# Optimization experiments

Hardware: AMD Instinct MI355X
Metric: run time of the kernel (lower is better)

The kernel has to match this reference:

```python
import jax, jax.numpy as jnp
import numpy as np

UNIF_T = 2.0
EPS = 1e-12  # matches F.normalize default eps


def _l2norm(a):
    return a / jnp.maximum(jnp.linalg.norm(a, axis=-1, keepdims=True), EPS)


def setup_inputs() -> dict:
    key = jax.random.key(0)
    k1, k2, k3, k4 = jax.random.split(key, 4)
    n, d = 2048, 512
    Q, K = 3, 8192
    n_classes = 16
    x = jax.random.normal(k1, (n, d), dtype=jnp.float32)
    q_data = jax.random.normal(k2, (Q, K, d), dtype=jnp.float32)
    targets = jax.random.randint(k3, (n,), 0, n_classes, dtype=jnp.int64)
    q_targets = jax.random.randint(k4, (Q, K), 0, n_classes, dtype=jnp.int64)
    return {"x": x, "q_data": q_data, "targets": targets, "q_targets": q_targets, "order": 1}


def reference(x, q_data, targets, q_targets, order):
    # x: [n, d], q_data: [Q, K, d], targets: [n], q_targets: [Q, K]
    Q, K, _ = q_data.shape
    xn = _l2norm(x)
    qn = _l2norm(q_data)
    sim = jnp.einsum('nd,qkd->qnk', xn, qn)      # [Q, n, K]
    e = jnp.exp(-UNIF_T * (2.0 - 2.0 * sim))     # [Q, n, K]
    # mask[i, j] = targets[i] == q_targets[order, j]; masked entries of the
    # `order` queue are excluded from that row's mean.
    mask = targets[:, None] == q_targets[order][None, :]   # [n, K] bool
    total = e.sum(axis=(0, 2))                              # [n]
    masked_sum = jnp.where(mask, e[order], 0.0).sum(axis=1) # [n]
    count = (Q * K - mask.sum(axis=1)).astype(e.dtype)      # [n]
    loss = jnp.mean(jnp.log((total - masked_sum) / count))
    return loss
```

## Files before the change

### kernel.cpp

```cpp
#include <hip/hip_runtime.h>
#include <cstdint>
#include <cstddef>

#define N_ROWS 2048
#define DIM    512
#define QN     3
#define KQ     8192
#define NCOL   (QN * KQ)
#define NCLASS 16

#define BM 256
#define BN 256
#define BKT 64
#define NT  (DIM / BKT)
#define NBLKP (NCOL / BN)

typedef __attribute__((ext_vector_type(4))) float f32x4;

__global__ __launch_bounds__(256) void norm_cast_kernel(
    const float* __restrict__ x, const float* __restrict__ q,
    unsigned char* __restrict__ xb, unsigned char* __restrict__ qb,
    float* __restrict__ out) {
    if (blockIdx.x == 0 && threadIdx.x == 0) out[0] = 0.f;
    int row = blockIdx.x * 4 + (threadIdx.x >> 6);
    int lane = threadIdx.x & 63;
    const float* src;
    unsigned char* dst;
    if (row < N_ROWS) {
        src = x + (size_t)row * DIM;
        dst = xb + (size_t)row * DIM;
    } else {
        src = q + (size_t)(row - N_ROWS) * DIM;
        dst = qb + (size_t)(row - N_ROWS) * DIM;
    }
    float4 v0 = ((const float4*)src)[lane * 2];
    float4 v1 = ((const float4*)src)[lane * 2 + 1];
    float ss = v0.x*v0.x + v0.y*v0.y + v0.z*v0.z + v0.w*v0.w
             + v1.x*v1.x + v1.y*v1.y + v1.z*v1.z + v1.w*v1.w;
    #pragma unroll
    for (int off = 1; off < 64; off <<= 1)
        ss += __shfl_xor(ss, off, 64);
    float inv = 16.0f / fmaxf(sqrtf(ss), 1e-12f);
    int w0 = __builtin_amdgcn_cvt_pk_fp8_f32(v0.x * inv, v0.y * inv, 0,  false);
    w0     = __builtin_amdgcn_cvt_pk_fp8_f32(v0.z * inv, v0.w * inv, w0, true);
    int w1 = __builtin_amdgcn_cvt_pk_fp8_f32(v1.x * inv, v1.y * inv, 0,  false);
    w1     = __builtin_amdgcn_cvt_pk_fp8_f32(v1.z * inv, v1.w * inv, w1, true);
    uint2 o; o.x = (unsigned)w0; o.y = (unsigned)w1;
    int r2 = (row >> 2) & 1;
    *(uint2*)(dst + ((lane * 8) ^ (r2 << 3))) = o;
}

#define MF(A_, B_, C_) C_ = __builtin_amdgcn_mfma_f32_16x16x32_fp8_fp8(A_, B_, C_, 0, 0, 0)

#define STAGE(h_) do {                                                          \
    const int t_ = (h_) >> 2, ht_ = (h_) & 3;                                   \
    const int chunk_ = (ht_ & 1) * 8 + wave;           \
    const int R_ = chunk_ * 16 + stR;                      \
    const int k0_ = t_ * BKT;                                                   \
    if (ht_ < 2) {                                                              \
        unsigned char* d_ = ((t_ & 1) ? As1 : As0) + chunk_ * 1024 + lane * 16; \
        __builtin_amdgcn_global_load_lds(                                       \
            (const __attribute__((address_space(1))) unsigned int*)             \
                (Xb + (size_t)(m0 + R_) * DIM + k0_ + stC),                     \
            (__attribute__((address_space(3))) unsigned int*)d_, 16, 0, 0);     \
    } else {                                                                    \
        unsigned char* d_ = ((t_ & 1) ? Bs1 : Bs0) + chunk_ * 1024 + lane * 16; \
        __builtin_amdgcn_global_load_lds(                                       \
            (const __attribute__((address_space(1))) unsigned int*)             \
                (Qb + (size_t)(n0 + R_) * DIM + k0_ + stC),                     \
            (__attribute__((address_space(3))) unsigned int*)d_, 16, 0, 0);     \
    }                                                                           \
} while (0)

__global__ __launch_bounds__(512) void gemm_epilogue_kernel(
    const unsigned char* __restrict__ Xb,
    const unsigned char* __restrict__ Qb,
    const int* __restrict__ targets,
    const int* __restrict__ q_targets,
    const int* __restrict__ order_p,
    float* __restrict__ P) {

    __shared__ unsigned char As0[BM * BKT];
    __shared__ unsigned char As1[BM * BKT];
    __shared__ unsigned char Bs0[BN * BKT];
    __shared__ unsigned char Bs1[BN * BKT];

    const int tid  = threadIdx.x;
    const int lane = tid & 63;
    const int wave = tid >> 6;
    const int wm = wave >> 2, wn = wave & 3;
    const int quad = lane >> 4;
    const int l15  = lane & 15;
    const int r2l  = (l15 >> 2) & 1;
    const int skey = ((l15 >> 1) & 1) * 2 + ((l15 >> 3) & 1);

    const int b    = blockIdx.x;
    const int xcd  = b & 7;
    const int g    = b >> 3;
    const int colb = (g >> 3) * 8 + xcd;
    const int rowb = g & 7;
    const int m0 = rowb * BM;
    const int n0 = colb * BN;

    f32x4 acc[8][4];
    #pragma unroll
    for (int i = 0; i < 8; i++)
        #pragma unroll
        for (int j = 0; j < 4; j++)
            acc[i][j] = (f32x4){0.f, 0.f, 0.f, 0.f};

    const int stR = lane >> 2;
    const int stC = ((lane & 3) ^ (((stR >> 1) & 1) * 2 + ((stR >> 3) & 1))) * 16;

    const int swh = ((quad & 1) ^ r2l) << 3;
    const int sw0 = ((((quad >> 1)    ) ^ skey) << 4) + swh;
    const int sw1 = ((((quad >> 1) + 2) ^ skey) << 4) + swh;

    #pragma unroll
    for (int h = 0; h < 7; ++h) STAGE(h);
    asm volatile("s_waitcnt vmcnt(3)" ::: "memory");
    __builtin_amdgcn_sched_barrier(0);
    __builtin_amdgcn_s_barrier();

    #pragma unroll
    for (int ph = 0; ph < 32; ++ph) {
        const int it = ph >> 3, p = ph & 7;
        const int tt = it * 2 + (p >> 2);
        const int q  = p & 3;
        const unsigned char* Ab = (tt & 1) ? As1 : As0;
        const unsigned char* Bb = (tt & 1) ? Bs1 : Bs0;
        const int mt0 = (q >> 1) * 4, ntb = (q & 1) * 2;

        long a0[2], a1[2], a2[2], a3[2], b0[2], b1[2];
        {
            const unsigned char* pA0 = Ab + (wm * 128 + (mt0 + 0) * 16 + l15) * BKT;
            const unsigned char* pA1 = Ab + (wm * 128 + (mt0 + 1) * 16 + l15) * BKT;
            const unsigned char* pA2 = Ab + (wm * 128 + (mt0 + 2) * 16 + l15) * BKT;
            const unsigned char* pA3 = Ab + (wm * 128 + (mt0 + 3) * 16 + l15) * BKT;
            a0[0] = *(const long*)(pA0 + sw0); a0[1] = *(const long*)(pA0 + sw1);
            a1[0] = *(const long*)(pA1 + sw0); a1[1] = *(const long*)(pA1 + sw1);
            a2[0] = *(const long*)(pA2 + sw0); a2[1] = *(const long*)(pA2 + sw1);
            a3[0] = *(const long*)(pA3 + sw0); a3[1] = *(const long*)(pA3 + sw1);
            const unsigned char* pB0 = Bb + (wn * 64 + (ntb + 0) * 16 + l15) * BKT;
            const unsigned char* pB1 = Bb + (wn * 64 + (ntb + 1) * 16 + l15) * BKT;
            b0[0] = *(const long*)(pB0 + sw0); b0[1] = *(const long*)(pB0 + sw1);
            b1[0] = *(const long*)(pB1 + sw0); b1[1] = *(const long*)(pB1 + sw1);
        }

        const int hs = 7 + ph;
        if (hs < 4 * NT) STAGE(hs);

        if (q == 3) {
            if (it == 3) asm volatile("s_waitcnt vmcnt(0)" ::: "memory");
            else         asm volatile("s_waitcnt vmcnt(3)" ::: "memory");
            __builtin_amdgcn_sched_barrier(0);
        }
        __builtin_amdgcn_s_barrier();

        __builtin_amdgcn_s_setprio(1);
        #pragma unroll
        for (int ks = 0; ks < 2; ++ks) {
            MF(a0[ks], b0[ks], acc[mt0 + 0][ntb + 0]);
            MF(a0[ks], b1[ks], acc[mt0 + 0][ntb + 1]);
            MF(a1[ks], b0[ks], acc[mt0 + 1][ntb + 0]);
            MF(a1[ks], b1[ks], acc[mt0 + 1][ntb + 1]);
            MF(a2[ks], b0[ks], acc[mt0 + 2][ntb + 0]);
            MF(a2[ks], b1[ks], acc[mt0 + 2][ntb + 1]);
            MF(a3[ks], b0[ks], acc[mt0 + 3][ntb + 0]);
            MF(a3[ks], b1[ks], acc[mt0 + 3][ntb + 1]);
        }
        __builtin_amdgcn_s_setprio(0);
        __builtin_amdgcn_s_barrier();
    }

    __syncthreads();
    float* red = (float*)&As0[0];

    const int ord  = order_p[0];
    const int qIdx = colb / (KQ / BN);
    const bool isOrd = (qIdx == ord);
    const int kbase = n0 - qIdx * KQ;

    int qtv[4] = {0, 0, 0, 0};
    if (isOrd) {
        #pragma unroll
        for (int nt = 0; nt < 4; nt++)
            qtv[nt] = q_targets[ord * KQ + kbase + wn * 64 + nt * 16 + l15];
    }

    #pragma unroll
    for (int mt = 0; mt < 8; mt++) {
        int rowl = wm * 128 + mt * 16 + quad * 4;
        int tg[4] = {0, 0, 0, 0};
        if (isOrd) {
            #pragma unroll
            for (int reg = 0; reg < 4; reg++) tg[reg] = targets[m0 + rowl + reg];
        }
        #pragma unroll
        for (int reg = 0; reg < 4; reg++) {
            float s = 0.f;
            #pragma unroll
            for (int nt = 0; nt < 4; nt++) {
                float v256 = acc[mt][nt][reg];
                float e = __expf(v256 * 0.015625f - 4.0f);
                if (isOrd && tg[reg] == qtv[nt]) e = 0.f;
                s += e;
            }
            s += __shfl_xor(s, 1, 64);
            s += __shfl_xor(s, 2, 64);
            s += __shfl_xor(s, 4, 64);
            s += __shfl_xor(s, 8, 64);
            if (l15 == 0)
                red[wn * 256 + rowl + reg] = s;
        }
    }
    __syncthreads();
    if (tid < 256)
        P[(size_t)colb * N_ROWS + m0 + tid] =
            red[tid] + red[256 + tid] + red[512 + tid] + red[768 + tid];
}

__global__ __launch_bounds__(256) void reduce_kernel(
    const float* __restrict__ P,
    const int* __restrict__ targets,
    const int* __restrict__ q_targets,
    const int* __restrict__ order_p,
    float* __restrict__ out) {
    __shared__ int hist[NCLASS];
    __shared__ float partial[4];
    int tid = threadIdx.x;
    int wave = tid >> 6, lane = tid & 63;
    if (tid < NCLASS) hist[tid] = 0;
    __syncthreads();
    int ord = order_p[0];

    int local[NCLASS];
    #pragma unroll
    for (int c = 0; c < NCLASS; c++) local[c] = 0;
    for (int i = tid; i < KQ; i += 256) {
        int v = q_targets[ord * KQ + i];
        #pragma unroll
        for (int c = 0; c < NCLASS; c++)
            local[c] += __popcll(__ballot(v == c));
    }
    if (lane == 0) {
        #pragma unroll
        for (int c = 0; c < NCLASS; c++)
            atomicAdd(&hist[c], local[c]);
    }
    __syncthreads();

    int r = blockIdx.x * 256 + tid;
    float total = 0.f;
    #pragma unroll 8
    for (int nb = 0; nb < NBLKP; nb++)
        total += P[(size_t)nb * N_ROWS + r];
    float cnt = (float)(QN * KQ - hist[targets[r]]);
    float v = logf(total / cnt);

    #pragma unroll
    for (int off = 1; off < 64; off <<= 1)
        v += __shfl_xor(v, off, 64);
    if (lane == 0) partial[wave] = v;
    __syncthreads();
    if (tid == 0)
        atomicAdd(out, (partial[0] + partial[1] + partial[2] + partial[3])
                       * (1.0f / (float)N_ROWS));
}

extern "C" void kernel_launch(void* const* d_in, const int* in_sizes, int n_in,
                              void* d_out, int out_size, void* d_ws, size_t ws_size,
                              hipStream_t stream) {
    const float* x         = (const float*)d_in[0];
    const float* q         = (const float*)d_in[1];
    const int*   targets   = (const int*)d_in[2];
    const int*   q_targets = (const int*)d_in[3];
    const int*   order     = (const int*)d_in[4];
    float* out = (float*)d_out;

    char* ws = (char*)d_ws;
    float* P = (float*)ws;
    unsigned char* Xb = (unsigned char*)(ws + (size_t)NBLKP * N_ROWS * 4);
    unsigned char* Qb = Xb + (size_t)N_ROWS * DIM;

    norm_cast_kernel<<<(N_ROWS + NCOL) / 4, 256, 0, stream>>>(x, q, Xb, Qb, out);

    gemm_epilogue_kernel<<<NBLKP * (N_ROWS / BM), 512, 0, stream>>>(
        Xb, Qb, targets, q_targets, order, P);

    reduce_kernel<<<N_ROWS / 256, 256, 0, stream>>>(P, targets, q_targets, order, out);
}
```

Baseline: 180.5 us.

## Restructure GEMM main loop into 16 larger phases with B fragments reused

Replaces the 32 small phases (each 8 MFMAs on a 4x2 sub-tile) with 16 phases of 32 MFMAs. Each K-tile's B fragments are loaded once into registers and reused across both M halves. This halves the number of block barriers and cuts redundant LDS reads of B, at the cost of more live registers. Two global-to-LDS stages are now issued per phase, which changes how the async copies and vmcnt waits are spaced.

```diff
diff --git a/kernel.cpp b/kernel.cpp
--- a/kernel.cpp
+++ b/kernel.cpp
@@ -72,6 +72,71 @@
     }                                                                           \
 } while (0)
 
+#define RD_A(AB, MT0) do {                                                      \
+    const unsigned char* p_;                                                    \
+    p_ = (AB) + (wm * 128 + ((MT0) + 0) * 16 + l15) * BKT;                      \
+    a0[0] = *(const long*)(p_ + sw0); a0[1] = *(const long*)(p_ + sw1);         \
+    p_ = (AB) + (wm * 128 + ((MT0) + 1) * 16 + l15) * BKT;                      \
+    a1[0] = *(const long*)(p_ + sw0); a1[1] = *(const long*)(p_ + sw1);         \
+    p_ = (AB) + (wm * 128 + ((MT0) + 2) * 16 + l15) * BKT;                      \
+    a2[0] = *(const long*)(p_ + sw0); a2[1] = *(const long*)(p_ + sw1);         \
+    p_ = (AB) + (wm * 128 + ((MT0) + 3) * 16 + l15) * BKT;                      \
+    a3[0] = *(const long*)(p_ + sw0); a3[1] = *(const long*)(p_ + sw1);         \
+} while (0)
+
+#define RD_B(BB) do {                                                           \
+    const unsigned char* p_;                                                    \
+    p_ = (BB) + (wn * 64 +  0 + l15) * BKT;                                     \
+    B0[0] = *(const long*)(p_ + sw0); B0[1] = *(const long*)(p_ + sw1);         \
+    p_ = (BB) + (wn * 64 + 16 + l15) * BKT;                                     \
+    B1[0] = *(const long*)(p_ + sw0); B1[1] = *(const long*)(p_ + sw1);         \
+    p_ = (BB) + (wn * 64 + 32 + l15) * BKT;                                     \
+    B2[0] = *(const long*)(p_ + sw0); B2[1] = *(const long*)(p_ + sw1);         \
+    p_ = (BB) + (wn * 64 + 48 + l15) * BKT;                                     \
+    B3[0] = *(const long*)(p_ + sw0); B3[1] = *(const long*)(p_ + sw1);         \
+} while (0)
+
+#define MFMA16(KS, MT0)                                                         \
+    MF(a0[KS], B0[KS], acc[(MT0)+0][0]); MF(a0[KS], B1[KS], acc[(MT0)+0][1]);   \
+    MF(a0[KS], B2[KS], acc[(MT0)+0][2]); MF(a0[KS], B3[KS], acc[(MT0)+0][3]);   \
+    MF(a1[KS], B0[KS], acc[(MT0)+1][0]); MF(a1[KS], B1[KS], acc[(MT0)+1][1]);   \
+    MF(a1[KS], B2[KS], acc[(MT0)+1][2]); MF(a1[KS], B3[KS], acc[(MT0)+1][3]);   \
+    MF(a2[KS], B0[KS], acc[(MT0)+2][0]); MF(a2[KS], B1[KS], acc[(MT0)+2][1]);   \
+    MF(a2[KS], B2[KS], acc[(MT0)+2][2]); MF(a2[KS], B3[KS], acc[(MT0)+2][3]);   \
+    MF(a3[KS], B0[KS], acc[(MT0)+3][0]); MF(a3[KS], B1[KS], acc[(MT0)+3][1]);   \
+    MF(a3[KS], B2[KS], acc[(MT0)+3][2]); MF(a3[KS], B3[KS], acc[(MT0)+3][3]);
+
+#define VM3 do { asm volatile("s_waitcnt vmcnt(3)" ::: "memory");               \
+                 __builtin_amdgcn_sched_barrier(0); } while (0)
+#define VM0 do { asm volatile("s_waitcnt vmcnt(0)" ::: "memory");               \
+                 __builtin_amdgcn_sched_barrier(0); } while (0)
+#define NOSTG ((void)0)
+
+#define PH_S0(AB, BB, S1_, S2_) do {                                            \
+    long a0[2], a1[2], a2[2], a3[2];                                            \
+    RD_A(AB, 0); RD_B(BB);                                                      \
+    __builtin_amdgcn_sched_barrier(0);                                          \
+    S1_; S2_;                                                                   \
+    __builtin_amdgcn_s_barrier();                                               \
+    __builtin_amdgcn_s_setprio(1);                                              \
+    MFMA16(0, 0) MFMA16(1, 0)                                                   \
+    __builtin_amdgcn_s_setprio(0);                                              \
+    __builtin_amdgcn_s_barrier();                                               \
+} while (0)
+
+#define PH_S1(AB, S1_, S2_, WAIT_) do {                                         \
+    long a0[2], a1[2], a2[2], a3[2];                                            \
+    RD_A(AB, 4);                                                                \
+    __builtin_amdgcn_sched_barrier(0);                                          \
+    S1_; S2_;                                                                   \
+    WAIT_;                                                                      \
+    __builtin_amdgcn_s_barrier();                                               \
+    __builtin_amdgcn_s_setprio(1);                                              \
+    MFMA16(0, 4) MFMA16(1, 4)                                                   \
+    __builtin_amdgcn_s_setprio(0);                                              \
+    __builtin_amdgcn_s_barrier();                                               \
+} while (0)
+
 __global__ __launch_bounds__(512) void gemm_epilogue_kernel(
     const unsigned char* __restrict__ Xb,
     const unsigned char* __restrict__ Qb,
@@ -116,62 +181,30 @@
     const int sw0 = ((((quad >> 1)    ) ^ skey) << 4) + swh;
     const int sw1 = ((((quad >> 1) + 2) ^ skey) << 4) + swh;
 
+    long B0[2], B1[2], B2[2], B3[2];
+
     #pragma unroll
     for (int h = 0; h < 7; ++h) STAGE(h);
     asm volatile("s_waitcnt vmcnt(3)" ::: "memory");
     __builtin_amdgcn_sched_barrier(0);
     __builtin_amdgcn_s_barrier();
 
-    #pragma unroll
-    for (int ph = 0; ph < 32; ++ph) {
-        const int it = ph >> 3, p = ph & 7;
-        const int tt = it * 2 + (p >> 2);
-        const int q  = p & 3;
-        const unsigned char* Ab = (tt & 1) ? As1 : As0;
-        const unsigned char* Bb = (tt & 1) ? Bs1 : Bs0;
-        const int mt0 = (q >> 1) * 4, ntb = (q & 1) * 2;
-
-        long a0[2], a1[2], a2[2], a3[2], b0[2], b1[2];
-        {
-            const unsigned char* pA0 = Ab + (wm * 128 + (mt0 + 0) * 16 + l15) * BKT;
-            const unsigned char* pA1 = Ab + (wm * 128 + (mt0 + 1) * 16 + l15) * BKT;
-            const unsigned char* pA2 = Ab + (wm * 128 + (mt0 + 2) * 16 + l15) * BKT;
-            const unsigned char* pA3 = Ab + (wm * 128 + (mt0 + 3) * 16 + l15) * BKT;
-            a0[0] = *(const long*)(pA0 + sw0); a0[1] = *(const long*)(pA0 + sw1);
-            a1[0] = *(const long*)(pA1 + sw0); a1[1] = *(const long*)(pA1 + sw1);
-            a2[0] = *(const long*)(pA2 + sw0); a2[1] = *(const long*)(pA2 + sw1);
-            a3[0] = *(const long*)(pA3 + sw0); a3[1] = *(const long*)(pA3 + sw1);
-            const unsigned char* pB0 = Bb + (wn * 64 + (ntb + 0) * 16 + l15) * BKT;
-            const unsigned char* pB1 = Bb + (wn * 64 + (ntb + 1) * 16 + l15) * BKT;
-            b0[0] = *(const long*)(pB0 + sw0); b0[1] = *(const long*)(pB0 + sw1);
-            b1[0] = *(const long*)(pB1 + sw0); b1[1] = *(const long*)(pB1 + sw1);
-        }
-
-        const int hs = 7 + ph;
-        if (hs < 4 * NT) STAGE(hs);
-
-        if (q == 3) {
-            if (it == 3) asm volatile("s_waitcnt vmcnt(0)" ::: "memory");
-            else         asm volatile("s_waitcnt vmcnt(3)" ::: "memory");
-            __builtin_amdgcn_sched_barrier(0);
-        }
-        __builtin_amdgcn_s_barrier();
-
-        __builtin_amdgcn_s_setprio(1);
-        #pragma unroll
-        for (int ks = 0; ks < 2; ++ks) {
-            MF(a0[ks], b0[ks], acc[mt0 + 0][ntb + 0]);
-            MF(a0[ks], b1[ks], acc[mt0 + 0][ntb + 1]);
-            MF(a1[ks], b0[ks], acc[mt0 + 1][ntb + 0]);
-            MF(a1[ks], b1[ks], acc[mt0 + 1][ntb + 1]);
-            MF(a2[ks], b0[ks], acc[mt0 + 2][ntb + 0]);
-            MF(a2[ks], b1[ks], acc[mt0 + 2][ntb + 1]);
-            MF(a3[ks], b0[ks], acc[mt0 + 3][ntb + 0]);
-            MF(a3[ks], b1[ks], acc[mt0 + 3][ntb + 1]);
-        }
-        __builtin_amdgcn_s_setprio(0);
-        __builtin_amdgcn_s_barrier();
-    }
+    PH_S0(As0, Bs0, STAGE(7),  STAGE(8));
+    PH_S1(As0,      STAGE(9),  STAGE(10), VM3);
+    PH_S0(As1, Bs1, STAGE(11), STAGE(12));
+    PH_S1(As1,      STAGE(13), STAGE(14), VM3);
+    PH_S0(As0, Bs0, STAGE(15), STAGE(16));
+    PH_S1(As0,      STAGE(17), STAGE(18), VM3);
+    PH_S0(As1, Bs1, STAGE(19), STAGE(20));
+    PH_S1(As1,      STAGE(21), STAGE(22), VM3);
+    PH_S0(As0, Bs0, STAGE(23), STAGE(24));
+    PH_S1(As0,      STAGE(25), STAGE(26), VM3);
+    PH_S0(As1, Bs1, STAGE(27), STAGE(28));
+    PH_S1(As1,      STAGE(29), STAGE(30), VM3);
+    PH_S0(As0, Bs0, STAGE(31), NOSTG);
+    PH_S1(As0,      NOSTG, NOSTG, VM0);
+    PH_S0(As1, Bs1, NOSTG, NOSTG);
+    PH_S1(As1,      NOSTG, NOSTG, NOSTG);
 
     __syncthreads();
     float* red = (float*)&As0[0];
```

Measured after the change: 170.1 us. 5.8% less time.
